# Kernel optimization log

Hardware: AMD Instinct MI355X
Metric: run time of the kernel (lower is better)

The kernel has to match this reference:

```python
import jax, jax.numpy as jnp
import numpy as np

B, S, C = 4, 2048, 1024
DK = C // 4   # 256, q/k projection dim
DO = 1024     # out_channels


def setup_inputs() -> dict:
    key = jax.random.key(0)
    ks = jax.random.split(key, 7)
    s = 1.0 / np.sqrt(C)
    return {
        "x": jax.random.normal(ks[0], (B, S, C), dtype=jnp.float32),
        "Wq": jax.random.uniform(ks[1], (C, DK), jnp.float32, -s, s),
        "bq": jax.random.uniform(ks[2], (DK,), jnp.float32, -s, s),
        "Wk": jax.random.uniform(ks[3], (C, DK), jnp.float32, -s, s),
        "bk": jax.random.uniform(ks[4], (DK,), jnp.float32, -s, s),
        "Wv": jax.random.uniform(ks[5], (C, DO), jnp.float32, -s, s),
        "bv": jax.random.uniform(ks[6], (DO,), jnp.float32, -s, s),
    }


def reference(x, Wq, bq, Wk, bk, Wv, bv):
    q = jnp.einsum("bsc,cd->bsd", x, Wq) + bq   # [B,S,DK]
    k = jnp.einsum("bsc,cd->bsd", x, Wk) + bk   # [B,S,DK]
    v = jnp.einsum("bsc,cd->bsd", x, Wv) + bv   # [B,S,DO]
    scores = jnp.einsum("bqd,bkd->bqk", q, k) / jnp.sqrt(jnp.float32(DK))
    attn = jax.nn.softmax(scores, axis=-1)      # [B,S,S]
    return jnp.einsum("bqk,bkd->bqd", attn, v)  # [B,S,DO]
```

## Files before the change

kernel.cpp:

```cpp
#include <hip/hip_runtime.h>
#include <hip/hip_bf16.h>

typedef __attribute__((ext_vector_type(8))) short short8;
typedef __attribute__((ext_vector_type(8))) __bf16 bf16x8;
typedef __attribute__((ext_vector_type(4))) float f32x4;

#define MFMA(a, b, c) __builtin_amdgcn_mfma_f32_16x16x32_bf16((a), (b), (c), 0, 0, 0)
#define SCALE 0.0625f

static __device__ __forceinline__ void gload16(const void* g, void* l) {
  __builtin_amdgcn_global_load_lds(
      (const __attribute__((address_space(1))) void*)g,
      (__attribute__((address_space(3))) void*)l, 16, 0, 0);
}

static __device__ __forceinline__ unsigned short f2b(float f) {
  union { __hip_bfloat16 h; unsigned short u; } cv;
  cv.h = __float2bfloat16(f);
  return cv.u;
}

__global__ __launch_bounds__(256) void convert_x_kern(const float* __restrict__ x,
                                                      unsigned short* __restrict__ xb) {
  long i = ((long)blockIdx.x * 256 + threadIdx.x) * 8;
  float4 a = *reinterpret_cast<const float4*>(x + i);
  float4 b = *reinterpret_cast<const float4*>(x + i + 4);
  short8 o;
  o[0] = (short)f2b(a.x); o[1] = (short)f2b(a.y); o[2] = (short)f2b(a.z); o[3] = (short)f2b(a.w);
  o[4] = (short)f2b(b.x); o[5] = (short)f2b(b.y); o[6] = (short)f2b(b.z); o[7] = (short)f2b(b.w);
  *reinterpret_cast<short8*>(xb + i) = o;
}

__global__ void pack_bias_kern(const float* __restrict__ bq, const float* __restrict__ bk,
                               const float* __restrict__ bv, float* __restrict__ bc) {
  int i = blockIdx.x * 256 + threadIdx.x;
  float v = (i < 256) ? bq[i] : (i < 512) ? bk[i - 256] : bv[i - 512];
  bc[i] = v;
}

__global__ __launch_bounds__(256) void transpose_w_kern(const float* __restrict__ src,
                                                        unsigned short* __restrict__ dst,
                                                        int ldsrc, int lddst) {
  __shared__ __align__(16) unsigned short tile[64][72];
  int r0 = blockIdx.y * 64, c0 = blockIdx.x * 64;
  int t = threadIdx.x;
  #pragma unroll
  for (int it = 0; it < 4; ++it) {
    int idx = it * 1024 + t * 4;
    int row = idx >> 6, col = idx & 63;
    float4 v = *reinterpret_cast<const float4*>(src + (long)(r0 + row) * ldsrc + c0 + col);
    tile[row][col + 0] = f2b(v.x); tile[row][col + 1] = f2b(v.y);
    tile[row][col + 2] = f2b(v.z); tile[row][col + 3] = f2b(v.w);
  }
  __syncthreads();
  #pragma unroll
  for (int it = 0; it < 4; ++it) {
    int idx = it * 1024 + t * 4;
    int orow = idx >> 6, ocol = idx & 63;
    ushort4 o;
    o.x = tile[ocol + 0][orow]; o.y = tile[ocol + 1][orow];
    o.z = tile[ocol + 2][orow]; o.w = tile[ocol + 3][orow];
    *reinterpret_cast<ushort4*>(dst + (long)(c0 + orow) * lddst + r0 + ocol) = o;
  }
}

template <int SWZ, int BN, bool BIAS, bool VSPLIT, bool EXPSUM>
__global__ __launch_bounds__(512, 2) void gemm_pi(
    const unsigned short* __restrict__ A, const unsigned short* __restrict__ B,
    const float* __restrict__ bias, void* __restrict__ Cout,
    int NT, int lda, int ldb, int ldc,
    long batchA, long batchB, long batchC,
    float* __restrict__ lpart,
    unsigned short* __restrict__ vT) {
  constexpr int WM = 128;
  constexpr int WN = BN / 4;
  constexpr int NF = BN / 64;
  constexpr int BR = BN / 64;
  constexpr int ASH = 256 * 64;
  constexpr int TSH = ASH + BN * 64;
  __shared__ __align__(128) unsigned short lds[2 * TSH];

  int bid = blockIdx.x;
  int b = 0, tm, tn;
  if constexpr (SWZ == 0) {
    int xcd = bid & 7, s = bid >> 3;
    tm = xcd * 4 + (s >> 3); tn = s & 7;
  } else {
    int xcd = bid & 7, s = bid >> 3;
    b = xcd >> 1; tm = (xcd & 1) * 4 + (s >> 3); tn = s & 7;
  }

  int t = threadIdx.x, w = t >> 6, l = t & 63;
  int wr = w >> 2, wc = w & 3;
  int g = l >> 4, c = l & 15;

  f32x4 acc[8][NF];
  #pragma unroll
  for (int m = 0; m < 8; ++m)
    #pragma unroll
    for (int n = 0; n < NF; ++n) acc[m][n] = (f32x4){0.f, 0.f, 0.f, 0.f};

  int srow = t >> 3;
  int scb = (t & 7) * 16;
  const unsigned short* aptr = A + (long)b * batchA + (long)(tm * 256) * lda;
  const unsigned short* bptr = B + (long)b * batchB + (long)(tn * BN) * ldb;
  int kb = scb ^ ((srow & 7) << 4);

  auto stageA = [&](int buf, int k0, int r) {
    int row = r * 64 + srow;
    gload16(aptr + (long)row * lda + k0 + (kb >> 1),
            lds + buf * TSH + r * 4096 + t * 8);
  };
  auto stageB = [&](int buf, int k0, int r) {
    int row = r * 64 + srow;
    gload16(bptr + (long)row * ldb + k0 + (kb >> 1),
            lds + buf * TSH + ASH + r * 4096 + t * 8);
  };
  auto ldA = [&](const char* abase, int mh, int kh, int m) {
    int row = wr * WM + mh * 64 + m * 16 + c;
    int pb = row * 128 + (kh * 32 + g * 8) * 2;
    pb ^= ((pb >> 7) & 7) << 4;
    return *reinterpret_cast<const bf16x8*>(abase + pb);
  };
  auto ldB = [&](const char* bbase, int kh, int n) {
    int row = wc * WN + n * 16 + c;
    int pb = row * 128 + (kh * 32 + g * 8) * 2;
    pb ^= ((pb >> 7) & 7) << 4;
    return *reinterpret_cast<const bf16x8*>(bbase + pb);
  };

  #pragma unroll
  for (int r = 0; r < BR; ++r) stageB(0, 0, r);
  stageA(0, 0, 0); stageA(0, 0, 2); stageA(0, 0, 1); stageA(0, 0, 3);
  asm volatile("s_waitcnt vmcnt(0)" ::: "memory");
  __builtin_amdgcn_s_barrier();

  for (int kt = 0; kt < NT; ++kt) {
    int cur = kt & 1, nb = cur ^ 1;
    const char* abase = (const char*)(lds + cur * TSH);
    const char* bbase = (const char*)(lds + cur * TSH + ASH);
    bool more = (kt + 1) < NT;
    int k1 = (kt + 1) * 64;
    bf16x8 bfr[NF];
    #pragma unroll
    for (int p = 0; p < 4; ++p) {
      const int kh = p >> 1, mh = p & 1;
      bf16x8 af[4];
      #pragma unroll
      for (int m = 0; m < 4; ++m) af[m] = ldA(abase, mh, kh, m);
      if (mh == 0) {
        #pragma unroll
        for (int n = 0; n < NF; ++n) bfr[n] = ldB(bbase, kh, n);
      }
      if (more) {
        if constexpr (BN == 256) {
          if      (p == 0) { stageB(nb, k1, 0); stageB(nb, k1, 1); }
          else if (p == 1) { stageB(nb, k1, 2); stageB(nb, k1, 3); }
          else if (p == 2) { stageA(nb, k1, 0); stageA(nb, k1, 2); }
          else             { stageA(nb, k1, 1); stageA(nb, k1, 3); }
        } else {
          if      (p == 0) { stageB(nb, k1, 0); stageB(nb, k1, 1); stageB(nb, k1, 2); }
          else if (p == 1) { stageA(nb, k1, 0); stageA(nb, k1, 2); }
          else if (p == 2) { stageA(nb, k1, 1); stageA(nb, k1, 3); }
        }
      }
      __builtin_amdgcn_s_barrier();
      asm volatile("s_waitcnt lgkmcnt(0)" ::: "memory");
      __builtin_amdgcn_sched_barrier(0);
      __builtin_amdgcn_s_setprio(1);
      #pragma unroll
      for (int m = 0; m < 4; ++m)
        #pragma unroll
        for (int n = 0; n < NF; ++n)
          acc[mh * 4 + m][n] = MFMA(af[m], bfr[n], acc[mh * 4 + m][n]);
      __builtin_amdgcn_s_setprio(0);
      if (p == 0) {
        if (kt == NT - 1) asm volatile("s_waitcnt vmcnt(0)" ::: "memory");
        else if (BN == 256) asm volatile("s_waitcnt vmcnt(2)" ::: "memory");
        else                asm volatile("s_waitcnt vmcnt(3)" ::: "memory");
      }
      if (p == 3 && more) {
        asm volatile("s_waitcnt vmcnt(2)" ::: "memory");
      }
      __builtin_amdgcn_s_barrier();
    }
  }

  int rbase = tm * 256 + wr * WM + g * 4;
  int c0 = tn * BN + wc * WN + c;

  if constexpr (EXPSUM) {
    __shared__ float lred[4][256];
    #pragma unroll
    for (int mi = 0; mi < 8; ++mi) {
      int roff = (mi / 4) * 64 + (mi % 4) * 16;
      #pragma unroll
      for (int j = 0; j < 4; ++j) {
        long ob = (long)b * batchC + (long)(rbase + roff + j) * ldc + c0;
        float rs = 0.f;
        #pragma unroll
        for (int n = 0; n < NF; ++n) {
          float pv = __expf(acc[mi][n][j] * SCALE);
          ((unsigned short*)Cout)[ob + n * 16] = f2b(pv);
          rs += pv;
        }
        rs += __shfl_xor(rs, 1); rs += __shfl_xor(rs, 2);
        rs += __shfl_xor(rs, 4); rs += __shfl_xor(rs, 8);
        if (c == 0) lred[wc][wr * WM + roff + g * 4 + j] = rs;
      }
    }
    __syncthreads();
    for (int rr = t; rr < 256; rr += 512) {
      float s = lred[0][rr] + lred[1][rr] + lred[2][rr] + lred[3][rr];
      lpart[((long)b * 2048 + tm * 256 + rr) * 8 + tn] = s;
    }
  } else {
    #pragma unroll
    for (int mi = 0; mi < 8; ++mi) {
      int roff = (mi / 4) * 64 + (mi % 4) * 16;
      int s0 = (rbase + roff) & 2047;
      #pragma unroll
      for (int n = 0; n < NF; ++n) {
        int col = c0 + n * 16;
        float bv = BIAS ? bias[col] : 0.f;
        if (VSPLIT && (col - c) >= 512) {
          int bb = tm >> 3;
          ushort4 pk;
          pk.x = f2b(acc[mi][n][0] + bv); pk.y = f2b(acc[mi][n][1] + bv);
          pk.z = f2b(acc[mi][n][2] + bv); pk.w = f2b(acc[mi][n][3] + bv);
          *reinterpret_cast<ushort4*>(vT + (long)bb * 2097152 +
                                      (long)(col - 512) * 2048 + s0) = pk;
        } else {
          long rowb = (long)b * batchC + (long)(rbase + roff) * ldc + col;
          #pragma unroll
          for (int j = 0; j < 4; ++j)
            ((unsigned short*)Cout)[rowb + (long)j * ldc] = f2b(acc[mi][n][j] + bv);
        }
      }
    }
  }
}

__global__ __launch_bounds__(512, 2) void gemm_pv(
    const unsigned short* __restrict__ A,
    const unsigned short* __restrict__ B,
    float* __restrict__ Cout,
    const float* __restrict__ linv) {
  constexpr int NT = 32;
  constexpr int ASH = 128 * 64;
  constexpr int TSH = ASH + 256 * 64;
  __shared__ __align__(128) unsigned short lds[3 * TSH];

  int bid = blockIdx.x;
  int xcd = bid & 7, sidx = bid >> 3;
  int b = xcd >> 1;
  int tm = (xcd & 1) * 8 + (sidx >> 2), tn = sidx & 3;

  int t = threadIdx.x, w = t >> 6, l = t & 63;
  int wr = w >> 2, wc = w & 3;
  int g = l >> 4, c = l & 15;

  f32x4 acc[4][4];
  #pragma unroll
  for (int m = 0; m < 4; ++m)
    #pragma unroll
    for (int n = 0; n < 4; ++n) acc[m][n] = (f32x4){0.f, 0.f, 0.f, 0.f};

  int srow = t >> 3;
  int scb = (t & 7) * 16;
  int kb = scb ^ ((srow & 7) << 4);
  const unsigned short* aptr = A + (long)b * 4194304 + (long)(tm * 128) * 2048;
  const unsigned short* bptr = B + (long)b * 2097152 + (long)(tn * 256) * 2048;

  auto stageA = [&](int buf, int k0) {
    #pragma unroll
    for (int r = 0; r < 2; ++r) {
      int row = r * 64 + srow;
      gload16(aptr + (long)row * 2048 + k0 + (kb >> 1),
              lds + buf * TSH + r * 4096 + t * 8);
    }
  };
  auto stageB = [&](int buf, int k0) {
    #pragma unroll
    for (int r = 0; r < 4; ++r) {
      int row = r * 64 + srow;
      gload16(bptr + (long)row * 2048 + k0 + (kb >> 1),
              lds + buf * TSH + ASH + r * 4096 + t * 8);
    }
  };

  stageA(0, 0); stageB(0, 0);
  stageA(1, 64); stageB(1, 64);
  asm volatile("s_waitcnt vmcnt(6)" ::: "memory");
  __builtin_amdgcn_s_barrier();

  for (int kt = 0; kt < NT; ++kt) {
    int cur = kt % 3, nxt = (kt + 2) % 3;
    const char* abase = (const char*)(lds + cur * TSH);
    const char* bbase = abase + ASH * 2;

    bf16x8 af[2][4], bf[2][4];
    #pragma unroll
    for (int sk = 0; sk < 2; ++sk) {
      #pragma unroll
      for (int m = 0; m < 4; ++m) {
        int p = (wr * 64 + m * 16 + c) * 128 + (sk * 32 + g * 8) * 2;
        p ^= ((p >> 7) & 7) << 4;
        af[sk][m] = *reinterpret_cast<const bf16x8*>(abase + p);
      }
      #pragma unroll
      for (int n = 0; n < 4; ++n) {
        int p = (wc * 64 + n * 16 + c) * 128 + (sk * 32 + g * 8) * 2;
        p ^= ((p >> 7) & 7) << 4;
        bf[sk][n] = *reinterpret_cast<const bf16x8*>(bbase + p);
      }
    }

    if (kt + 2 < NT) {
      int k2 = (kt + 2) * 64;
      stageA(nxt, k2); stageB(nxt, k2);
    }

    __builtin_amdgcn_s_setprio(1);
    #pragma unroll
    for (int sk = 0; sk < 2; ++sk)
      #pragma unroll
      for (int m = 0; m < 4; ++m)
        #pragma unroll
        for (int n = 0; n < 4; ++n)
          acc[m][n] = MFMA(af[sk][m], bf[sk][n], acc[m][n]);
    __builtin_amdgcn_s_setprio(0);

    if (kt < NT - 1) {
      if (kt == NT - 2) asm volatile("s_waitcnt vmcnt(0)" ::: "memory");
      else              asm volatile("s_waitcnt vmcnt(6)" ::: "memory");
      __builtin_amdgcn_s_barrier();
    }
  }

  int rbase = tm * 128 + wr * 64 + g * 4;
  int c0 = tn * 256 + wc * 64 + c;
  #pragma unroll
  for (int mi = 0; mi < 4; ++mi) {
    float lv[4];
    #pragma unroll
    for (int j = 0; j < 4; ++j)
      lv[j] = linv[(long)b * 2048 + rbase + mi * 16 + j];
    #pragma unroll
    for (int n = 0; n < 4; ++n) {
      long rowb = (long)b * 2097152 + (long)(rbase + mi * 16) * 1024 + c0 + n * 16;
      #pragma unroll
      for (int j = 0; j < 4; ++j)
        Cout[rowb + (long)j * 1024] = acc[mi][n][j] * lv[j];
    }
  }
}

__global__ __launch_bounds__(256) void linv_kern(const float* __restrict__ lpart,
                                                 float* __restrict__ linv) {
  int r = blockIdx.x * 256 + threadIdx.x;
  float s = 0.f;
  #pragma unroll
  for (int i = 0; i < 8; ++i) s += lpart[(long)r * 8 + i];
  linv[r] = 1.f / s;
}

extern "C" void kernel_launch(void* const* d_in, const int* in_sizes, int n_in,
                              void* d_out, int out_size, void* d_ws, size_t ws_size,
                              hipStream_t stream) {
  (void)in_sizes; (void)n_in; (void)out_size; (void)ws_size;
  const float* x  = (const float*)d_in[0];
  const float* Wq = (const float*)d_in[1];
  const float* bq = (const float*)d_in[2];
  const float* Wk = (const float*)d_in[3];
  const float* bk = (const float*)d_in[4];
  const float* Wv = (const float*)d_in[5];
  const float* bv = (const float*)d_in[6];
  float* out = (float*)d_out;
  char* ws = (char*)d_ws;

  unsigned short* xb   = (unsigned short*)(ws + 0);
  float*          lpart= (float*)         (ws + 0);
  float*          linv = (float*)         (ws + 262144);
  unsigned short* wt   = (unsigned short*)(ws + 16777216);
  float*          bc   = (float*)         (ws + 19922944);
  unsigned short* qkv  = (unsigned short*)(ws + 19929088);
  unsigned short* vT   = (unsigned short*)(ws + 45094912);
  unsigned short* attn = (unsigned short*)(ws + 61872128);

  convert_x_kern<<<4096, 256, 0, stream>>>(x, xb);
  pack_bias_kern<<<6, 256, 0, stream>>>(bq, bk, bv, bc);
  transpose_w_kern<<<dim3(4, 16), 256, 0, stream>>>(Wq, wt,              256, 1024);
  transpose_w_kern<<<dim3(4, 16), 256, 0, stream>>>(Wk, wt + 256 * 1024, 256, 1024);
  transpose_w_kern<<<dim3(16, 16), 256, 0, stream>>>(Wv, wt + 512 * 1024, 1024, 1024);

  gemm_pi<0, 192, true, true, false><<<dim3(256), 512, 0, stream>>>(
      xb, wt, bc, qkv, 16, 1024, 1024, 1536, 0, 0, 0, nullptr, vT);

  gemm_pi<1, 256, false, false, true><<<dim3(256), 512, 0, stream>>>(
      qkv, qkv + 256, nullptr, attn, 4, 1536, 1536, 2048,
      (long)2048 * 1536, (long)2048 * 1536, (long)2048 * 2048, lpart, nullptr);
  linv_kern<<<32, 256, 0, stream>>>(lpart, linv);

  gemm_pv<<<dim3(256), 512, 0, stream>>>(attn, vT, out, linv);
}
```

Baseline: 109.5 us.

## Merge prep kernels into one launch and run PV GEMM with 1024-thread blocks

Replaces the five preprocessing launches (x conversion, bias packing, three weight transposes) with one prep kernel that dispatches on block index. The PV GEMM now runs 16 waves per block instead of 8, so each wave owns 32 rows rather than 64. Staging work is split so each thread issues 3 async loads per k-step instead of 6. This cuts launch overhead and per-wave register pressure in exchange for more waves competing for LDS and barriers. The launch_bounds(1024,4) hint may be unattainable given the 3-stage LDS buffer size.

```diff
diff --git a/kernel.cpp b/kernel.cpp
--- a/kernel.cpp
+++ b/kernel.cpp
@@ -20,30 +20,38 @@
   return cv.u;
 }
 
-__global__ __launch_bounds__(256) void convert_x_kern(const float* __restrict__ x,
-                                                      unsigned short* __restrict__ xb) {
-  long i = ((long)blockIdx.x * 256 + threadIdx.x) * 8;
-  float4 a = *reinterpret_cast<const float4*>(x + i);
-  float4 b = *reinterpret_cast<const float4*>(x + i + 4);
-  short8 o;
-  o[0] = (short)f2b(a.x); o[1] = (short)f2b(a.y); o[2] = (short)f2b(a.z); o[3] = (short)f2b(a.w);
-  o[4] = (short)f2b(b.x); o[5] = (short)f2b(b.y); o[6] = (short)f2b(b.z); o[7] = (short)f2b(b.w);
-  *reinterpret_cast<short8*>(xb + i) = o;
-}
-
-__global__ void pack_bias_kern(const float* __restrict__ bq, const float* __restrict__ bk,
-                               const float* __restrict__ bv, float* __restrict__ bc) {
-  int i = blockIdx.x * 256 + threadIdx.x;
-  float v = (i < 256) ? bq[i] : (i < 512) ? bk[i - 256] : bv[i - 512];
-  bc[i] = v;
-}
-
-__global__ __launch_bounds__(256) void transpose_w_kern(const float* __restrict__ src,
-                                                        unsigned short* __restrict__ dst,
-                                                        int ldsrc, int lddst) {
+__global__ __launch_bounds__(256) void prep_kern(
+    const float* __restrict__ x, unsigned short* __restrict__ xb,
+    const float* __restrict__ bq, const float* __restrict__ bk,
+    const float* __restrict__ bv, float* __restrict__ bc,
+    const float* __restrict__ Wq, const float* __restrict__ Wk,
+    const float* __restrict__ Wv, unsigned short* __restrict__ wt) {
   __shared__ __align__(16) unsigned short tile[64][72];
-  int r0 = blockIdx.y * 64, c0 = blockIdx.x * 64;
-  int t = threadIdx.x;
+  int bid = blockIdx.x, t = threadIdx.x;
+  if (bid < 4096) {
+    long i = ((long)bid * 256 + t) * 8;
+    float4 a = *reinterpret_cast<const float4*>(x + i);
+    float4 b = *reinterpret_cast<const float4*>(x + i + 4);
+    short8 o;
+    o[0] = (short)f2b(a.x); o[1] = (short)f2b(a.y); o[2] = (short)f2b(a.z); o[3] = (short)f2b(a.w);
+    o[4] = (short)f2b(b.x); o[5] = (short)f2b(b.y); o[6] = (short)f2b(b.z); o[7] = (short)f2b(b.w);
+    *reinterpret_cast<short8*>(xb + i) = o;
+    return;
+  }
+  if (bid < 4102) {
+    int i = (bid - 4096) * 256 + t;
+    float v = (i < 256) ? bq[i] : (i < 512) ? bk[i - 256] : bv[i - 512];
+    bc[i] = v;
+    return;
+  }
+  const float* src; unsigned short* dst; int ldsrc, lam;
+  if (bid < 4166)      { lam = bid - 4102; src = Wq; dst = wt;              ldsrc = 256;
+                         lam = (lam & 3) | ((lam >> 2) << 8); }
+  else if (bid < 4230) { lam = bid - 4166; src = Wk; dst = wt + 256 * 1024; ldsrc = 256;
+                         lam = (lam & 3) | ((lam >> 2) << 8); }
+  else                 { lam = bid - 4230; src = Wv; dst = wt + 512 * 1024; ldsrc = 1024;
+                         lam = (lam & 15) | ((lam >> 4) << 8); }
+  int c0 = (lam & 255) * 64, r0 = (lam >> 8) * 64;
   #pragma unroll
   for (int it = 0; it < 4; ++it) {
     int idx = it * 1024 + t * 4;
@@ -60,7 +68,7 @@
     ushort4 o;
     o.x = tile[ocol + 0][orow]; o.y = tile[ocol + 1][orow];
     o.z = tile[ocol + 2][orow]; o.w = tile[ocol + 3][orow];
-    *reinterpret_cast<ushort4*>(dst + (long)(c0 + orow) * lddst + r0 + ocol) = o;
+    *reinterpret_cast<ushort4*>(dst + (long)(c0 + orow) * 1024 + r0 + ocol) = o;
   }
 }
 
@@ -241,7 +249,7 @@
   }
 }
 
-__global__ __launch_bounds__(512, 2) void gemm_pv(
+__global__ __launch_bounds__(1024, 4) void gemm_pv(
     const unsigned short* __restrict__ A,
     const unsigned short* __restrict__ B,
     float* __restrict__ Cout,
@@ -260,9 +268,9 @@
   int wr = w >> 2, wc = w & 3;
   int g = l >> 4, c = l & 15;
 
-  f32x4 acc[4][4];
-  #pragma unroll
-  for (int m = 0; m < 4; ++m)
+  f32x4 acc[2][4];
+  #pragma unroll
+  for (int m = 0; m < 2; ++m)
     #pragma unroll
     for (int n = 0; n < 4; ++n) acc[m][n] = (f32x4){0.f, 0.f, 0.f, 0.f};
 
@@ -272,39 +280,32 @@
   const unsigned short* aptr = A + (long)b * 4194304 + (long)(tm * 128) * 2048;
   const unsigned short* bptr = B + (long)b * 2097152 + (long)(tn * 256) * 2048;
 
-  auto stageA = [&](int buf, int k0) {
+  auto stage3 = [&](int buf, int kt2) {
+    int k0 = kt2 * 64;
+    gload16(aptr + (long)srow * 2048 + k0 + (kb >> 1),
+            lds + buf * TSH + t * 8);
     #pragma unroll
     for (int r = 0; r < 2; ++r) {
-      int row = r * 64 + srow;
-      gload16(aptr + (long)row * 2048 + k0 + (kb >> 1),
-              lds + buf * TSH + r * 4096 + t * 8);
+      int row = r * 128 + srow;
+      gload16(bptr + (long)row * 2048 + k0 + (kb >> 1),
+              lds + buf * TSH + ASH + r * 8192 + t * 8);
     }
   };
-  auto stageB = [&](int buf, int k0) {
-    #pragma unroll
-    for (int r = 0; r < 4; ++r) {
-      int row = r * 64 + srow;
-      gload16(bptr + (long)row * 2048 + k0 + (kb >> 1),
-              lds + buf * TSH + ASH + r * 4096 + t * 8);
-    }
-  };
-
-  stageA(0, 0); stageB(0, 0);
-  stageA(1, 64); stageB(1, 64);
-  asm volatile("s_waitcnt vmcnt(6)" ::: "memory");
+
+  stage3(0, 0); stage3(1, 1);
+  asm volatile("s_waitcnt vmcnt(3)" ::: "memory");
   __builtin_amdgcn_s_barrier();
 
   for (int kt = 0; kt < NT; ++kt) {
-    int cur = kt % 3, nxt = (kt + 2) % 3;
-    const char* abase = (const char*)(lds + cur * TSH);
+    const char* abase = (const char*)(lds + (kt % 3) * TSH);
     const char* bbase = abase + ASH * 2;
 
-    bf16x8 af[2][4], bf[2][4];
+    bf16x8 af[2][2], bf[2][4];
     #pragma unroll
     for (int sk = 0; sk < 2; ++sk) {
       #pragma unroll
-      for (int m = 0; m < 4; ++m) {
-        int p = (wr * 64 + m * 16 + c) * 128 + (sk * 32 + g * 8) * 2;
+      for (int m = 0; m < 2; ++m) {
+        int p = (wr * 32 + m * 16 + c) * 128 + (sk * 32 + g * 8) * 2;
         p ^= ((p >> 7) & 7) << 4;
         af[sk][m] = *reinterpret_cast<const bf16x8*>(abase + p);
       }
@@ -316,16 +317,13 @@
       }
     }
 
-    if (kt + 2 < NT) {
-      int k2 = (kt + 2) * 64;
-      stageA(nxt, k2); stageB(nxt, k2);
-    }
+    if (kt + 2 < NT) stage3((kt + 2) % 3, kt + 2);
 
     __builtin_amdgcn_s_setprio(1);
     #pragma unroll
     for (int sk = 0; sk < 2; ++sk)
       #pragma unroll
-      for (int m = 0; m < 4; ++m)
+      for (int m = 0; m < 2; ++m)
         #pragma unroll
         for (int n = 0; n < 4; ++n)
           acc[m][n] = MFMA(af[sk][m], bf[sk][n], acc[m][n]);
@@ -333,15 +331,15 @@
 
     if (kt < NT - 1) {
       if (kt == NT - 2) asm volatile("s_waitcnt vmcnt(0)" ::: "memory");
-      else              asm volatile("s_waitcnt vmcnt(6)" ::: "memory");
+      else              asm volatile("s_waitcnt vmcnt(3)" ::: "memory");
       __builtin_amdgcn_s_barrier();
     }
   }
 
-  int rbase = tm * 128 + wr * 64 + g * 4;
+  int rbase = tm * 128 + wr * 32 + g * 4;
   int c0 = tn * 256 + wc * 64 + c;
   #pragma unroll
-  for (int mi = 0; mi < 4; ++mi) {
+  for (int mi = 0; mi < 2; ++mi) {
     float lv[4];
     #pragma unroll
     for (int j = 0; j < 4; ++j)
@@ -388,11 +386,7 @@
   unsigned short* vT   = (unsigned short*)(ws + 45094912);
   unsigned short* attn = (unsigned short*)(ws + 61872128);
 
-  convert_x_kern<<<4096, 256, 0, stream>>>(x, xb);
-  pack_bias_kern<<<6, 256, 0, stream>>>(bq, bk, bv, bc);
-  transpose_w_kern<<<dim3(4, 16), 256, 0, stream>>>(Wq, wt,              256, 1024);
-  transpose_w_kern<<<dim3(4, 16), 256, 0, stream>>>(Wk, wt + 256 * 1024, 256, 1024);
-  transpose_w_kern<<<dim3(16, 16), 256, 0, stream>>>(Wv, wt + 512 * 1024, 1024, 1024);
+  prep_kern<<<4486, 256, 0, stream>>>(x, xb, bq, bk, bv, bc, Wq, Wk, Wv, wt);
 
   gemm_pi<0, 192, true, true, false><<<dim3(256), 512, 0, stream>>>(
       xb, wt, bc, qkv, 16, 1024, 1024, 1536, 0, 0, 0, nullptr, vT);
@@ -402,5 +396,5 @@
       (long)2048 * 1536, (long)2048 * 1536, (long)2048 * 2048, lpart, nullptr);
   linv_kern<<<32, 256, 0, stream>>>(lpart, linv);
 
-  gemm_pv<<<dim3(256), 512, 0, stream>>>(attn, vT, out, linv);
-}
+  gemm_pv<<<dim3(256), 1024, 0, stream>>>(attn, vT, out, linv);
+}
```

After: 101.5 us. 1.08x faster.
